# Kernel tuning notes

Hardware: AMD Instinct MI355X
Metric: run time of the kernel (lower is better)

Reference implementation:

```python
import jax, jax.numpy as jnp
import numpy as np

N_POINTS = 1048576
N_LEVELS = 16
F = 2
BASE_RES = 16
FINEST_RES = 512
LOG2_HASH = 19
SIZES = [2 ** min(i + 1, LOG2_HASH) for i in range(N_LEVELS)]  # per-level table rows (powers of 2)
OFFS = np.concatenate([[0], np.cumsum(SIZES)]).astype(np.int64)  # static row offsets into packed table
TOTAL_ROWS = int(OFFS[-1])  # 131070
# hash primes from the torch module; uint32 wraparound matches int64 low-bit behavior
# because each table size is a power of two <= 2^19 < 2^32, so h % 2^k == low k bits.
P0, P1, P2, P3 = np.uint32(1), np.uint32(2654435761), np.uint32(29675113), np.uint32(123456789)
CORNERS = np.array([[0,0,0],[1,0,0],[0,1,0],[1,1,0],
                    [0,0,1],[1,0,1],[0,1,1],[1,1,1]], dtype=np.uint32)  # torch stacking order


def setup_inputs() -> dict:
    key = jax.random.key(0)
    k1, k2 = jax.random.split(key)
    coords = jax.random.uniform(k1, (N_POINTS, 3), dtype=jnp.float32, minval=-1.0, maxval=1.0)
    hash_init_scale = 0.001
    table = jax.random.uniform(k2, (TOTAL_ROWS, F), dtype=jnp.float32,
                               minval=-hash_init_scale, maxval=hash_init_scale)
    return {"coords": coords, "table": table}


def _encode(coords, table):
    corners = jnp.asarray(CORNERS)  # [8,3] uint32
    outs = []
    for level in range(N_LEVELS):
        res = min(BASE_RES * (2 ** level), FINEST_RES)
        cs = (coords + 1.0) * res           # [N,3]
        cf = jnp.floor(cs)
        frac = cs - cf                      # [N,3]
        base = cf.astype(jnp.uint32)        # coords >= -1 so floor >= 0
        c = base[None, :, :] + corners[:, None, :]   # [8,N,3]
        x, y, z = c[..., 0], c[..., 1], c[..., 2]
        h = x * P0
        h = h * P1 + y
        h = h * P2 + z
        h = h * P3
        h = (h & jnp.uint32(SIZES[level] - 1)).astype(jnp.int32)  # mod power-of-2 table size
        feats = table[int(OFFS[level]) + h]          # [8,N,F] gather
        tx = frac[..., 0:1]; ty = frac[..., 1:2]; tz = frac[..., 2:3]
        f = (feats[0] * (1 - tx) * (1 - ty) * (1 - tz)
             + feats[1] * tx * (1 - ty) * (1 - tz)
             + feats[2] * (1 - tx) * ty * (1 - tz)
             + feats[3] * tx * ty * (1 - tz)
             + feats[4] * (1 - tx) * (1 - ty) * tz
             + feats[5] * tx * (1 - ty) * tz
             + feats[6] * (1 - tx) * ty * tz
             + feats[7] * tx * ty * tz)              # [N,F]
        outs.append(f)
    return jnp.concatenate(outs, axis=-1)            # [N, N_LEVELS*F]


def reference(coords, table):
    return _encode(coords, table)
```

## Files before the change

### kernel.cpp

```cpp
#include <hip/hip_runtime.h>


#define N_POINTS 1048576
#define N_LEVELS 16
#define BLOCK 1024
#define STAGED_ROWS 16382
#define STAGED_BYTES (STAGED_ROWS * 8)

__global__ __launch_bounds__(BLOCK) void ngp_encode_kernel(
    const float* __restrict__ coords,
    const float* __restrict__ table,
    float* __restrict__ out)
{
    extern __shared__ float2 lds_tb[];

    {
        float4* __restrict__ l4 = (float4*)lds_tb;
        const float4* __restrict__ t4 = (const float4*)table;
        const int n4 = STAGED_BYTES / 16;
        for (int idx = threadIdx.x; idx < n4; idx += BLOCK)
            l4[idx] = t4[idx];
    }
    __syncthreads();

    const int i = blockIdx.x * BLOCK + threadIdx.x;

    const float px = coords[3 * i + 0];
    const float py = coords[3 * i + 1];
    const float pz = coords[3 * i + 2];

    constexpr unsigned P1 = 2654435761u, P2 = 29675113u, P3 = 123456789u;
    constexpr unsigned HA = P1 * P2 * P3;
    constexpr unsigned HB = P2 * P3;
    constexpr unsigned HC = P3;

    const float2* __restrict__ tb = (const float2*)table;

    float res_out[2 * N_LEVELS];

#pragma unroll
    for (int l = 0; l < N_LEVELS; ++l) {
        int res_i = 16 << l;
        if (res_i > 512) res_i = 512;
        const float fres = (float)res_i;

        const float csx = (px + 1.0f) * fres;
        const float csy = (py + 1.0f) * fres;
        const float csz = (pz + 1.0f) * fres;
        const float cfx = floorf(csx);
        const float cfy = floorf(csy);
        const float cfz = floorf(csz);
        const float tx = csx - cfx;
        const float ty = csy - cfy;
        const float tz = csz - cfz;
        const unsigned bx = (unsigned)cfx;
        const unsigned by = (unsigned)cfy;
        const unsigned bz = (unsigned)cfz;

        const unsigned mask = (2u << l) - 1u;
        const unsigned off  = (2u << l) - 2u;

        const unsigned h000 = bx * HA + by * HB + bz * HC;

        float2 f000, f100, f010, f110, f001, f101, f011, f111;
        if (l <= 12) {
            f000 = lds_tb[off + ((h000) & mask)];
            f100 = lds_tb[off + ((h000 + HA) & mask)];
            f010 = lds_tb[off + ((h000 + HB) & mask)];
            f110 = lds_tb[off + ((h000 + HA + HB) & mask)];
            f001 = lds_tb[off + ((h000 + HC) & mask)];
            f101 = lds_tb[off + ((h000 + HA + HC) & mask)];
            f011 = lds_tb[off + ((h000 + HB + HC) & mask)];
            f111 = lds_tb[off + ((h000 + HA + HB + HC) & mask)];
        } else {
            f000 = tb[off + ((h000) & mask)];
            f100 = tb[off + ((h000 + HA) & mask)];
            f010 = tb[off + ((h000 + HB) & mask)];
            f110 = tb[off + ((h000 + HA + HB) & mask)];
            f001 = tb[off + ((h000 + HC) & mask)];
            f101 = tb[off + ((h000 + HA + HC) & mask)];
            f011 = tb[off + ((h000 + HB + HC) & mask)];
            f111 = tb[off + ((h000 + HA + HB + HC) & mask)];
        }

        const float ux = 1.0f - tx, uy = 1.0f - ty, uz = 1.0f - tz;
        const float w000 = ux * uy * uz;
        const float w100 = tx * uy * uz;
        const float w010 = ux * ty * uz;
        const float w110 = tx * ty * uz;
        const float w001 = ux * uy * tz;
        const float w101 = tx * uy * tz;
        const float w011 = ux * ty * tz;
        const float w111 = tx * ty * tz;

        float o0 = f000.x * w000 + f100.x * w100 + f010.x * w010 + f110.x * w110
                 + f001.x * w001 + f101.x * w101 + f011.x * w011 + f111.x * w111;
        float o1 = f000.y * w000 + f100.y * w100 + f010.y * w010 + f110.y * w110
                 + f001.y * w001 + f101.y * w101 + f011.y * w011 + f111.y * w111;

        res_out[2 * l + 0] = o0;
        res_out[2 * l + 1] = o1;
    }

    float4* __restrict__ o4 = (float4*)(out + (size_t)i * 32);
#pragma unroll
    for (int k = 0; k < 8; ++k) {
        o4[k] = make_float4(res_out[4 * k + 0], res_out[4 * k + 1],
                            res_out[4 * k + 2], res_out[4 * k + 3]);
    }
}

extern "C" void kernel_launch(void* const* d_in, const int* in_sizes, int n_in,
                              void* d_out, int out_size, void* d_ws, size_t ws_size,
                              hipStream_t stream) {
    const float* coords = (const float*)d_in[0];
    const float* table  = (const float*)d_in[1];
    float* out = (float*)d_out;

    hipFuncSetAttribute((const void*)ngp_encode_kernel,
                        hipFuncAttributeMaxDynamicSharedMemorySize,
                        STAGED_BYTES);

    const int grid = N_POINTS / BLOCK;
    ngp_encode_kernel<<<grid, BLOCK, STAGED_BYTES, stream>>>(coords, table, out);
}
```

Before: 248.9 us.

## Store staged hash table as fp16 in LDS and share hashes across levels

```diff
diff --git a/kernel.cpp b/kernel.cpp
--- a/kernel.cpp
+++ b/kernel.cpp
@@ -1,25 +1,38 @@
 #include <hip/hip_runtime.h>
+#include <hip/hip_fp16.h>
 
 
 #define N_POINTS 1048576
-#define N_LEVELS 16
 #define BLOCK 1024
 #define STAGED_ROWS 16382
-#define STAGED_BYTES (STAGED_ROWS * 8)
+#define STAGED_BYTES (STAGED_ROWS * 4)
 
-__global__ __launch_bounds__(BLOCK) void ngp_encode_kernel(
+__device__ __forceinline__ float2 ldsRow(const unsigned* __restrict__ lds, unsigned idx) {
+    unsigned u = lds[idx];
+    __half2 h = *(__half2*)&u;
+    return __half22float2(h);
+}
+
+__global__ __launch_bounds__(BLOCK, 8) void ngp_encode_kernel(
     const float* __restrict__ coords,
     const float* __restrict__ table,
     float* __restrict__ out)
 {
-    extern __shared__ float2 lds_tb[];
+    extern __shared__ unsigned lds_tb[];
 
     {
-        float4* __restrict__ l4 = (float4*)lds_tb;
         const float4* __restrict__ t4 = (const float4*)table;
-        const int n4 = STAGED_BYTES / 16;
-        for (int idx = threadIdx.x; idx < n4; idx += BLOCK)
-            l4[idx] = t4[idx];
+        uint2* __restrict__ l2 = (uint2*)lds_tb;
+        const int n = STAGED_ROWS / 2;
+        for (int r = threadIdx.x; r < n; r += BLOCK) {
+            float4 v = t4[r];
+            __half2 a = __floats2half2_rn(v.x, v.y);
+            __half2 b = __floats2half2_rn(v.z, v.w);
+            uint2 u;
+            u.x = *(unsigned*)&a;
+            u.y = *(unsigned*)&b;
+            l2[r] = u;
+        }
     }
     __syncthreads();
 
@@ -33,71 +46,80 @@
     constexpr unsigned HA = P1 * P2 * P3;
     constexpr unsigned HB = P2 * P3;
     constexpr unsigned HC = P3;
+    const unsigned D[8] = {0u, HA, HB, HA + HB, HC, HA + HC, HB + HC, HA + HB + HC};
 
     const float2* __restrict__ tb = (const float2*)table;
 
-    float res_out[2 * N_LEVELS];
+    float res_out[32];
 
 #pragma unroll
-    for (int l = 0; l < N_LEVELS; ++l) {
-        int res_i = 16 << l;
-        if (res_i > 512) res_i = 512;
-        const float fres = (float)res_i;
-
+    for (int l = 0; l < 5; ++l) {
+        const float fres = (float)(16 << l);
         const float csx = (px + 1.0f) * fres;
         const float csy = (py + 1.0f) * fres;
         const float csz = (pz + 1.0f) * fres;
-        const float cfx = floorf(csx);
-        const float cfy = floorf(csy);
-        const float cfz = floorf(csz);
-        const float tx = csx - cfx;
-        const float ty = csy - cfy;
-        const float tz = csz - cfz;
-        const unsigned bx = (unsigned)cfx;
-        const unsigned by = (unsigned)cfy;
-        const unsigned bz = (unsigned)cfz;
-
+        const float cfx = floorf(csx), cfy = floorf(csy), cfz = floorf(csz);
+        const float tx = csx - cfx, ty = csy - cfy, tz = csz - cfz;
+        const unsigned h000 = (unsigned)cfx * HA + (unsigned)cfy * HB + (unsigned)cfz * HC;
+        const float ux = 1.0f - tx, uy = 1.0f - ty, uz = 1.0f - tz;
+        const float w[8] = {ux*uy*uz, tx*uy*uz, ux*ty*uz, tx*ty*uz,
+                            ux*uy*tz, tx*uy*tz, ux*ty*tz, tx*ty*tz};
         const unsigned mask = (2u << l) - 1u;
         const unsigned off  = (2u << l) - 2u;
+        float o0 = 0.0f, o1 = 0.0f;
+#pragma unroll
+        for (int c = 0; c < 8; ++c) {
+            float2 f = ldsRow(lds_tb, off + ((h000 + D[c]) & mask));
+            o0 += f.x * w[c];
+            o1 += f.y * w[c];
+        }
+        res_out[2 * l + 0] = o0;
+        res_out[2 * l + 1] = o1;
+    }
 
-        const unsigned h000 = bx * HA + by * HB + bz * HC;
+    float w5[8];
+    unsigned H[8];
+    {
+        const float fres = 512.0f;
+        const float csx = (px + 1.0f) * fres;
+        const float csy = (py + 1.0f) * fres;
+        const float csz = (pz + 1.0f) * fres;
+        const float cfx = floorf(csx), cfy = floorf(csy), cfz = floorf(csz);
+        const float tx = csx - cfx, ty = csy - cfy, tz = csz - cfz;
+        const unsigned h000 = (unsigned)cfx * HA + (unsigned)cfy * HB + (unsigned)cfz * HC;
+        const float ux = 1.0f - tx, uy = 1.0f - ty, uz = 1.0f - tz;
+        w5[0] = ux*uy*uz; w5[1] = tx*uy*uz; w5[2] = ux*ty*uz; w5[3] = tx*ty*uz;
+        w5[4] = ux*uy*tz; w5[5] = tx*uy*tz; w5[6] = ux*ty*tz; w5[7] = tx*ty*tz;
+#pragma unroll
+        for (int c = 0; c < 8; ++c) H[c] = h000 + D[c];
+    }
 
-        float2 f000, f100, f010, f110, f001, f101, f011, f111;
-        if (l <= 12) {
-            f000 = lds_tb[off + ((h000) & mask)];
-            f100 = lds_tb[off + ((h000 + HA) & mask)];
-            f010 = lds_tb[off + ((h000 + HB) & mask)];
-            f110 = lds_tb[off + ((h000 + HA + HB) & mask)];
-            f001 = lds_tb[off + ((h000 + HC) & mask)];
-            f101 = lds_tb[off + ((h000 + HA + HC) & mask)];
-            f011 = lds_tb[off + ((h000 + HB + HC) & mask)];
-            f111 = lds_tb[off + ((h000 + HA + HB + HC) & mask)];
-        } else {
-            f000 = tb[off + ((h000) & mask)];
-            f100 = tb[off + ((h000 + HA) & mask)];
-            f010 = tb[off + ((h000 + HB) & mask)];
-            f110 = tb[off + ((h000 + HA + HB) & mask)];
-            f001 = tb[off + ((h000 + HC) & mask)];
-            f101 = tb[off + ((h000 + HA + HC) & mask)];
-            f011 = tb[off + ((h000 + HB + HC) & mask)];
-            f111 = tb[off + ((h000 + HA + HB + HC) & mask)];
+#pragma unroll
+    for (int l = 5; l <= 12; ++l) {
+        const unsigned mask = (2u << l) - 1u;
+        const unsigned off  = (2u << l) - 2u;
+        float o0 = 0.0f, o1 = 0.0f;
+#pragma unroll
+        for (int c = 0; c < 8; ++c) {
+            float2 f = ldsRow(lds_tb, off + (H[c] & mask));
+            o0 += f.x * w5[c];
+            o1 += f.y * w5[c];
         }
+        res_out[2 * l + 0] = o0;
+        res_out[2 * l + 1] = o1;
+    }
 
-        const float ux = 1.0f - tx, uy = 1.0f - ty, uz = 1.0f - tz;
-        const float w000 = ux * uy * uz;
-        const float w100 = tx * uy * uz;
-        const float w010 = ux * ty * uz;
-        const float w110 = tx * ty * uz;
-        const float w001 = ux * uy * tz;
-        const float w101 = tx * uy * tz;
-        const float w011 = ux * ty * tz;
-        const float w111 = tx * ty * tz;
-
-        float o0 = f000.x * w000 + f100.x * w100 + f010.x * w010 + f110.x * w110
-                 + f001.x * w001 + f101.x * w101 + f011.x * w011 + f111.x * w111;
-        float o1 = f000.y * w000 + f100.y * w100 + f010.y * w010 + f110.y * w110
-                 + f001.y * w001 + f101.y * w101 + f011.y * w011 + f111.y * w111;
-
+#pragma unroll
+    for (int l = 13; l <= 15; ++l) {
+        const unsigned mask = (2u << l) - 1u;
+        const unsigned off  = (2u << l) - 2u;
+        float o0 = 0.0f, o1 = 0.0f;
+#pragma unroll
+        for (int c = 0; c < 8; ++c) {
+            float2 f = tb[off + (H[c] & mask)];
+            o0 += f.x * w5[c];
+            o1 += f.y * w5[c];
+        }
         res_out[2 * l + 0] = o0;
         res_out[2 * l + 1] = o1;
     }
```

After: 253.8 us. Within noise of the previous version (+2.0%).
